# Optimization experiments

Measured on AMD Instinct MI355X. Metric: run time of the kernel, lower is better.

Reference implementation:

```python
import jax, jax.numpy as jnp
import numpy as np

B, D = 8, 256
N_LIVE, K_NEW = 10000, 32
KC = N_LIVE + K_NEW
N_SAMPLES = 100
EPSILON = 0.1


def setup_inputs() -> dict:
    key = jax.random.key(0)
    k1, k2, k3, k4, k5, k6 = jax.random.split(key, 6)
    return {
        "xt": jax.random.normal(k1, (B, D), dtype=jnp.float32),
        "live_x0": jax.random.normal(k2, (B, N_LIVE, D), dtype=jnp.float32),
        "live_ll": jax.random.normal(k3, (B, N_LIVE, 1), dtype=jnp.float32),
        "x0": jax.random.normal(k4, (B, K_NEW, D), dtype=jnp.float32),
        "ll": jax.random.normal(k5, (B, K_NEW, 1), dtype=jnp.float32),
        "t_scale": jnp.float32(0.5),
        "boot_idx": jax.random.randint(k6, (N_SAMPLES, B, KC), 0, KC, dtype=jnp.int32),
    }


def reference(xt, live_x0, live_ll, x0, ll, t_scale, boot_idx):
    # --- spotlight_score core math ---
    # gaussian correction for the new particles: 0.5*||x0-xt||^2/sigma^2 + log(sigma)
    diff_new = x0 - xt[:, None, :]                                   # [B,K,D]
    corr_new = 0.5 * jnp.sum(diff_new ** 2, axis=-1, keepdims=True) / t_scale ** 2  # [B,K,1]
    current_x0 = jnp.concatenate([live_x0, x0], axis=1)              # [B,Kc,D]
    current_ll = jnp.concatenate(
        [live_ll, ll + corr_new + jnp.log(t_scale)], axis=1)         # [B,Kc,1]

    diff = current_x0 - xt[:, None, :]                               # [B,Kc,D]
    use_ll = (current_ll
              - 0.5 * jnp.sum(diff ** 2, axis=-1, keepdims=True) / t_scale ** 2
              - jnp.log(t_scale))                                    # [B,Kc,1]

    scores_p = diff / t_scale                                        # [B,Kc,D] per-particle scores
    logits = use_ll[..., 0]                                          # [B,Kc]

    # --- check_convergence: bootstrap resampled softmax reductions ---
    def body(carry, idx_n):                                          # idx_n: [B,Kc]
        s = jnp.take_along_axis(scores_p, idx_n[:, :, None], axis=1)  # [B,Kc,D]
        l = jnp.take_along_axis(logits, idx_n, axis=1)                # [B,Kc]
        w = jax.nn.softmax(l, axis=1)
        return carry, jnp.einsum('bk,bkd->bd', w, s)                  # [B,D]

    _, boot = jax.lax.scan(body, None, boot_idx)                      # [N,B,D]
    sigma_v = jnp.std(boot, axis=0, ddof=1)                           # [B,D] (torch.std is unbiased)
    converged = jnp.all(sigma_v < EPSILON * t_scale, axis=1)          # [B]

    # --- final importance-weighted score ---
    w = jax.nn.softmax(logits, axis=1)                                # [B,Kc]
    score = jnp.einsum('bk,bkd->bd', w, scores_p)                     # [B,D]
    return score, converged
```

## Files before the change

kernel.cpp:

```cpp
#include <hip/hip_runtime.h>
#include <math.h>

#define B 8
#define D 256
#define N_LIVE 10000
#define K_NEW 32
#define KC 10032
#define NS 100
#define NROW 101
#define EPS 0.1f
#define CAP 1024
#define ACT_CUT 87.0f
#define LBLK 314
#define BMAX_STRIDE 320

#define WS_HDR    0
#define WS_BMAX   160
#define WS_LOGITS (WS_BMAX + B * BMAX_STRIDE)
#define WS_ACTE   (WS_LOGITS + B * KC)
#define WS_ACTI   (WS_ACTE + B * CAP)
#define WS_LUT    (WS_ACTI + B * CAP)
#define WS_BOOT   (WS_LUT + B * KC / 2)

__global__ __launch_bounds__(256) void k_logits(
    const float* __restrict__ xt, const float* __restrict__ live_x0,
    const float* __restrict__ live_ll, const float* __restrict__ x0n,
    const float* __restrict__ lln, const float* __restrict__ ts_p,
    float* __restrict__ logits, float* __restrict__ bmax) {
  int b = blockIdx.y;
  int w = threadIdx.x >> 6;
  int lane = threadIdx.x & 63;
  int k0 = blockIdx.x * 32 + w * 8;
  bool valid = (k0 < KC);
  int kb = valid ? k0 : 0;
  float4 c = ((const float4*)(xt + b * D))[lane];

  float s[8];
#pragma unroll
  for (int p = 0; p < 8; p++) {
    int k = kb + p;
    const float* src = (k < N_LIVE)
        ? (live_x0 + ((size_t)b * N_LIVE + k) * D)
        : (x0n + ((size_t)b * K_NEW + (k - N_LIVE)) * D);
    float4 v = ((const float4*)src)[lane];
    float dx = v.x - c.x, dy = v.y - c.y, dz = v.z - c.z, dw = v.w - c.w;
    s[p] = dx * dx + dy * dy + dz * dz + dw * dw;
  }
#pragma unroll
  for (int off = 32; off; off >>= 1) {
#pragma unroll
    for (int p = 0; p < 8; p++) s[p] += __shfl_xor(s[p], off);
  }
  __shared__ float wlog[4];
  if (lane == 0) {
    float ts = *ts_p;
    float inv2 = 0.5f / (ts * ts), lts = logf(ts);
    float o[8];
#pragma unroll
    for (int p = 0; p < 8; p++) {
      int k = kb + p;
      o[p] = (k < N_LIVE)
          ? live_ll[(size_t)b * N_LIVE + k] - s[p] * inv2 - lts
          : lln[(size_t)b * K_NEW + (k - N_LIVE)];
    }
    if (valid) {
      float4 o0 = {o[0], o[1], o[2], o[3]}, o1 = {o[4], o[5], o[6], o[7]};
      *(float4*)(logits + (size_t)b * KC + kb) = o0;
      *(float4*)(logits + (size_t)b * KC + kb + 4) = o1;
      float m = fmaxf(fmaxf(fmaxf(o[0], o[1]), fmaxf(o[2], o[3])),
                      fmaxf(fmaxf(o[4], o[5]), fmaxf(o[6], o[7])));
      wlog[w] = m;
    } else {
      wlog[w] = -INFINITY;
    }
  }
  __syncthreads();
  if (threadIdx.x == 0)
    bmax[b * BMAX_STRIDE + blockIdx.x] =
        fmaxf(fmaxf(wlog[0], wlog[1]), fmaxf(wlog[2], wlog[3]));
}

__global__ __launch_bounds__(256) void k_bmax(
    const float* __restrict__ bmax, float* __restrict__ hdr) {
  int b = blockIdx.x;
  int tid = threadIdx.x;
  float m = -INFINITY;
  for (int i = tid; i < LBLK; i += 256) m = fmaxf(m, bmax[b * BMAX_STRIDE + i]);
#pragma unroll
  for (int off = 32; off; off >>= 1) m = fmaxf(m, __shfl_xor(m, off));
  __shared__ float sm[4];
  if ((tid & 63) == 0) sm[tid >> 6] = m;
  __syncthreads();
  if (tid == 0)
    hdr[b * 16] = fmaxf(fmaxf(sm[0], sm[1]), fmaxf(sm[2], sm[3]));
}

__global__ __launch_bounds__(256) void k_select(
    const float* __restrict__ logits, const float* __restrict__ hdrM,
    unsigned* __restrict__ hdr, float* __restrict__ act_e,
    int* __restrict__ act_idx, unsigned short* __restrict__ lut) {
  int b = blockIdx.y;
  int tid = blockIdx.x * 256 + threadIdx.x;
  float M = hdrM[b * 16];
  const float* lg = logits + (size_t)b * KC;
  int* cnt = (int*)&hdr[128 + b];
  for (int k = tid; k < KC; k += 8 * 256) {
    float l = lg[k];
    unsigned short v = 0;
    if (l > M - ACT_CUT) {
      int pos = atomicAdd(cnt, 1);
      if (pos < CAP) {
        act_e[b * CAP + pos] = expf(l - M);
        act_idx[b * CAP + pos] = k;
        v = (unsigned short)(pos + 1);
      }
    }
    lut[(size_t)b * KC + k] = v;
  }
}

__global__ __launch_bounds__(256) void k_boot(
    const float* __restrict__ live_x0, const float* __restrict__ x0n,
    const float* __restrict__ act_e, const int* __restrict__ act_idx,
    const unsigned* __restrict__ hdr, const unsigned short* __restrict__ lut,
    const int* __restrict__ boot_idx, float* __restrict__ boot) {
  int n = blockIdx.x;
  int b = blockIdx.y;
  int tid = threadIdx.x;
  int nw = tid >> 6, lane = tid & 63;
  __shared__ int cnt[CAP];
  __shared__ float wval[CAP];
  __shared__ int widx[CAP];
  __shared__ float4 part[4][64];
  __shared__ int snnz;
  __shared__ float sden[4];
  int A = min((int)hdr[128 + b], CAP);
  for (int i = tid; i < A; i += 256) cnt[i] = 0;
  if (tid == 0) snnz = 0;
  __syncthreads();

  if (n < NS) {
    const int4* row = (const int4*)(boot_idx + ((size_t)n * B + b) * KC);
    const unsigned short* lutb = lut + (size_t)b * KC;
    for (int k = tid; k < KC / 4; k += 256) {
      int4 v = row[k];
      int t;
      t = lutb[v.x]; if (t) atomicAdd(&cnt[t - 1], 1);
      t = lutb[v.y]; if (t) atomicAdd(&cnt[t - 1], 1);
      t = lutb[v.z]; if (t) atomicAdd(&cnt[t - 1], 1);
      t = lutb[v.w]; if (t) atomicAdd(&cnt[t - 1], 1);
    }
  } else {
    for (int i = tid; i < A; i += 256) cnt[i] = 1;
  }
  __syncthreads();

  float dpart = 0.f;
  for (int i = tid; i < A; i += 256) {
    int c = cnt[i];
    if (c) {
      float w = (float)c * act_e[b * CAP + i];
      int pos = atomicAdd(&snnz, 1);
      wval[pos] = w;
      widx[pos] = act_idx[b * CAP + i];
      dpart += w;
    }
  }
#pragma unroll
  for (int off = 32; off; off >>= 1) dpart += __shfl_xor(dpart, off);
  if ((tid & 63) == 0) sden[tid >> 6] = dpart;
  __syncthreads();
  float inv = 1.f / (sden[0] + sden[1] + sden[2] + sden[3]);
  int nnz = snnz;

  const float* lx = live_x0 + (size_t)b * N_LIVE * D;
  const float* nx = x0n + (size_t)b * K_NEW * D;
  float4 a0 = {0.f, 0.f, 0.f, 0.f}, a1 = {0.f, 0.f, 0.f, 0.f};
  int p = nw;
  for (; p + 4 < nnz; p += 8) {
    int j0 = widx[p], j1 = widx[p + 4];
    float w0 = wval[p], w1 = wval[p + 4];
    const float4* r0 = (const float4*)((j0 < N_LIVE) ? (lx + (size_t)j0 * D)
                                                     : (nx + (size_t)(j0 - N_LIVE) * D));
    const float4* r1 = (const float4*)((j1 < N_LIVE) ? (lx + (size_t)j1 * D)
                                                     : (nx + (size_t)(j1 - N_LIVE) * D));
    float4 v0 = r0[lane], v1 = r1[lane];
    a0.x = fmaf(w0, v0.x, a0.x); a0.y = fmaf(w0, v0.y, a0.y);
    a0.z = fmaf(w0, v0.z, a0.z); a0.w = fmaf(w0, v0.w, a0.w);
    a1.x = fmaf(w1, v1.x, a1.x); a1.y = fmaf(w1, v1.y, a1.y);
    a1.z = fmaf(w1, v1.z, a1.z); a1.w = fmaf(w1, v1.w, a1.w);
  }
  if (p < nnz) {
    int j = widx[p];
    float w = wval[p];
    const float4* r = (const float4*)((j < N_LIVE) ? (lx + (size_t)j * D)
                                                   : (nx + (size_t)(j - N_LIVE) * D));
    float4 v = r[lane];
    a0.x = fmaf(w, v.x, a0.x); a0.y = fmaf(w, v.y, a0.y);
    a0.z = fmaf(w, v.z, a0.z); a0.w = fmaf(w, v.w, a0.w);
  }
  a0.x += a1.x; a0.y += a1.y; a0.z += a1.z; a0.w += a1.w;
  part[nw][lane] = a0;
  __syncthreads();
  if (nw == 0) {
    float4 q0 = part[0][lane], q1 = part[1][lane], q2 = part[2][lane], q3 = part[3][lane];
    float4 r;
    r.x = ((q0.x + q1.x) + (q2.x + q3.x)) * inv;
    r.y = ((q0.y + q1.y) + (q2.y + q3.y)) * inv;
    r.z = ((q0.z + q1.z) + (q2.z + q3.z)) * inv;
    r.w = ((q0.w + q1.w) + (q2.w + q3.w)) * inv;
    ((float4*)(boot + ((size_t)b * NROW + n) * D))[lane] = r;
  }
}

__global__ __launch_bounds__(256) void k_final(
    const float* __restrict__ boot, const float* __restrict__ xt,
    const float* __restrict__ ts_p, float* __restrict__ out) {
  int b = blockIdx.x;
  int d = threadIdx.x;
  float ts = *ts_p;
  const float* bb = boot + (size_t)b * NROW * D + d;
  float sum = 0.f;
#pragma unroll 4
  for (int n = 0; n < NS; n++) sum += bb[(size_t)n * D];
  float mean = sum / (float)NS;
  float vs = 0.f;
#pragma unroll 4
  for (int n = 0; n < NS; n++) { float t = bb[(size_t)n * D] - mean; vs += t * t; }
  float sigma_raw = sqrtf(vs / (float)(NS - 1));
  bool ok = (sigma_raw / ts) < (EPS * ts);
  out[(size_t)b * D + d] = (bb[(size_t)NS * D] - xt[(size_t)b * D + d]) / ts;
  unsigned long long m = __ballot(ok);
  __shared__ int wok[4];
  if ((d & 63) == 0) wok[d >> 6] = (m == 0xFFFFFFFFFFFFFFFFull) ? 1 : 0;
  __syncthreads();
  if (d == 0) out[(size_t)B * D + b] = (wok[0] & wok[1] & wok[2] & wok[3]) ? 1.0f : 0.0f;
}

extern "C" void kernel_launch(void* const* d_in, const int* in_sizes, int n_in,
                              void* d_out, int out_size, void* d_ws, size_t ws_size,
                              hipStream_t stream) {
  const float* xt       = (const float*)d_in[0];
  const float* live_x0  = (const float*)d_in[1];
  const float* live_ll  = (const float*)d_in[2];
  const float* x0n      = (const float*)d_in[3];
  const float* lln      = (const float*)d_in[4];
  const float* ts_p     = (const float*)d_in[5];
  const int*   boot_idx = (const int*)d_in[6];
  float* out = (float*)d_out;
  float* ws  = (float*)d_ws;

  float* hdrM              = ws + WS_HDR;
  unsigned* hdr            = (unsigned*)(ws + WS_HDR);
  float* bmax              = ws + WS_BMAX;
  float* logits            = ws + WS_LOGITS;
  float* act_e             = ws + WS_ACTE;
  int*   act_idx           = (int*)(ws + WS_ACTI);
  unsigned short* lut      = (unsigned short*)(ws + WS_LUT);
  float* boot              = ws + WS_BOOT;

  hipMemsetAsync(hdr, 0, 160 * sizeof(unsigned), stream);

  k_logits<<<dim3(LBLK, B), 256, 0, stream>>>(xt, live_x0, live_ll, x0n, lln, ts_p, logits, bmax);
  k_bmax<<<dim3(B), 256, 0, stream>>>(bmax, hdrM);
  k_select<<<dim3(8, B), 256, 0, stream>>>(logits, hdrM, hdr, act_e, act_idx, lut);
  k_boot<<<dim3(NROW, B), 256, 0, stream>>>(live_x0, x0n, act_e, act_idx, hdr, lut, boot_idx, boot);
  k_final<<<dim3(B), 256, 0, stream>>>(boot, xt, ts_p, out);
}
```

Measured before the change: 191.6 us.

## Drop memset and bmax kernel, stage LUT in LDS, widen final reduction

Removes the hipMemsetAsync by zeroing the counter inside k_logits. It also removes k_bmax by having every k_select block recompute the per-batch max from the block maxima. k_boot now copies the per-batch LUT into shared memory before the gather, so the random lookups hit LDS instead of global memory, at the cost of about 20KB more LDS per block. k_final splits the sample loop across 1024 threads with a shared-memory reduction to shorten its serial latency.

```diff
diff --git a/kernel.cpp b/kernel.cpp
--- a/kernel.cpp
+++ b/kernel.cpp
@@ -26,8 +26,10 @@
     const float* __restrict__ xt, const float* __restrict__ live_x0,
     const float* __restrict__ live_ll, const float* __restrict__ x0n,
     const float* __restrict__ lln, const float* __restrict__ ts_p,
-    float* __restrict__ logits, float* __restrict__ bmax) {
+    float* __restrict__ logits, float* __restrict__ bmax,
+    unsigned* __restrict__ hdr) {
   int b = blockIdx.y;
+  if (blockIdx.x == 0 && threadIdx.x == 0) hdr[128 + b] = 0;
   int w = threadIdx.x >> 6;
   int lane = threadIdx.x & 63;
   int k0 = blockIdx.x * 32 + w * 8;
@@ -67,9 +69,8 @@
       float4 o0 = {o[0], o[1], o[2], o[3]}, o1 = {o[4], o[5], o[6], o[7]};
       *(float4*)(logits + (size_t)b * KC + kb) = o0;
       *(float4*)(logits + (size_t)b * KC + kb + 4) = o1;
-      float m = fmaxf(fmaxf(fmaxf(o[0], o[1]), fmaxf(o[2], o[3])),
+      wlog[w] = fmaxf(fmaxf(fmaxf(o[0], o[1]), fmaxf(o[2], o[3])),
                       fmaxf(fmaxf(o[4], o[5]), fmaxf(o[6], o[7])));
-      wlog[w] = m;
     } else {
       wlog[w] = -INFINITY;
     }
@@ -80,28 +81,22 @@
         fmaxf(fmaxf(wlog[0], wlog[1]), fmaxf(wlog[2], wlog[3]));
 }
 
-__global__ __launch_bounds__(256) void k_bmax(
-    const float* __restrict__ bmax, float* __restrict__ hdr) {
-  int b = blockIdx.x;
-  int tid = threadIdx.x;
-  float m = -INFINITY;
-  for (int i = tid; i < LBLK; i += 256) m = fmaxf(m, bmax[b * BMAX_STRIDE + i]);
-#pragma unroll
-  for (int off = 32; off; off >>= 1) m = fmaxf(m, __shfl_xor(m, off));
-  __shared__ float sm[4];
-  if ((tid & 63) == 0) sm[tid >> 6] = m;
-  __syncthreads();
-  if (tid == 0)
-    hdr[b * 16] = fmaxf(fmaxf(sm[0], sm[1]), fmaxf(sm[2], sm[3]));
-}
-
 __global__ __launch_bounds__(256) void k_select(
-    const float* __restrict__ logits, const float* __restrict__ hdrM,
+    const float* __restrict__ logits, const float* __restrict__ bmax,
     unsigned* __restrict__ hdr, float* __restrict__ act_e,
     int* __restrict__ act_idx, unsigned short* __restrict__ lut) {
   int b = blockIdx.y;
+  __shared__ float sm[4];
+  float m = -INFINITY;
+  for (int i = threadIdx.x; i < LBLK; i += 256)
+    m = fmaxf(m, bmax[b * BMAX_STRIDE + i]);
+#pragma unroll
+  for (int off = 32; off; off >>= 1) m = fmaxf(m, __shfl_xor(m, off));
+  if ((threadIdx.x & 63) == 0) sm[threadIdx.x >> 6] = m;
+  __syncthreads();
+  float M = fmaxf(fmaxf(sm[0], sm[1]), fmaxf(sm[2], sm[3]));
+
   int tid = blockIdx.x * 256 + threadIdx.x;
-  float M = hdrM[b * 16];
   const float* lg = logits + (size_t)b * KC;
   int* cnt = (int*)&hdr[128 + b];
   for (int k = tid; k < KC; k += 8 * 256) {
@@ -128,6 +123,7 @@
   int b = blockIdx.y;
   int tid = threadIdx.x;
   int nw = tid >> 6, lane = tid & 63;
+  __shared__ unsigned short slut[KC];
   __shared__ int cnt[CAP];
   __shared__ float wval[CAP];
   __shared__ int widx[CAP];
@@ -137,18 +133,22 @@
   int A = min((int)hdr[128 + b], CAP);
   for (int i = tid; i < A; i += 256) cnt[i] = 0;
   if (tid == 0) snnz = 0;
+  if (n < NS) {
+    const unsigned* src = (const unsigned*)(lut + (size_t)b * KC);
+    unsigned* dst = (unsigned*)slut;
+    for (int i = tid; i < KC / 2; i += 256) dst[i] = src[i];
+  }
   __syncthreads();
 
   if (n < NS) {
     const int4* row = (const int4*)(boot_idx + ((size_t)n * B + b) * KC);
-    const unsigned short* lutb = lut + (size_t)b * KC;
     for (int k = tid; k < KC / 4; k += 256) {
       int4 v = row[k];
       int t;
-      t = lutb[v.x]; if (t) atomicAdd(&cnt[t - 1], 1);
-      t = lutb[v.y]; if (t) atomicAdd(&cnt[t - 1], 1);
-      t = lutb[v.z]; if (t) atomicAdd(&cnt[t - 1], 1);
-      t = lutb[v.w]; if (t) atomicAdd(&cnt[t - 1], 1);
+      t = slut[v.x]; if (t) atomicAdd(&cnt[t - 1], 1);
+      t = slut[v.y]; if (t) atomicAdd(&cnt[t - 1], 1);
+      t = slut[v.z]; if (t) atomicAdd(&cnt[t - 1], 1);
+      t = slut[v.w]; if (t) atomicAdd(&cnt[t - 1], 1);
     }
   } else {
     for (int i = tid; i < A; i += 256) cnt[i] = 1;
@@ -213,28 +213,45 @@
   }
 }
 
-__global__ __launch_bounds__(256) void k_final(
+__global__ __launch_bounds__(1024) void k_final(
     const float* __restrict__ boot, const float* __restrict__ xt,
     const float* __restrict__ ts_p, float* __restrict__ out) {
   int b = blockIdx.x;
-  int d = threadIdx.x;
+  int tid = threadIdx.x;
+  int d = tid & 255;
+  int st = tid >> 8;
   float ts = *ts_p;
   const float* bb = boot + (size_t)b * NROW * D + d;
-  float sum = 0.f;
-#pragma unroll 4
-  for (int n = 0; n < NS; n++) sum += bb[(size_t)n * D];
-  float mean = sum / (float)NS;
+  __shared__ float red[4][256];
+  __shared__ float mrow[256];
+  __shared__ int wok[4];
+  float s = 0.f;
+#pragma unroll 5
+  for (int i = 0; i < 25; i++) s += bb[(size_t)(st + 4 * i) * D];
+  red[st][d] = s;
+  __syncthreads();
+  if (st == 0) mrow[d] = (red[0][d] + red[1][d] + red[2][d] + red[3][d]) / (float)NS;
+  __syncthreads();
+  float mean = mrow[d];
   float vs = 0.f;
-#pragma unroll 4
-  for (int n = 0; n < NS; n++) { float t = bb[(size_t)n * D] - mean; vs += t * t; }
-  float sigma_raw = sqrtf(vs / (float)(NS - 1));
-  bool ok = (sigma_raw / ts) < (EPS * ts);
-  out[(size_t)b * D + d] = (bb[(size_t)NS * D] - xt[(size_t)b * D + d]) / ts;
-  unsigned long long m = __ballot(ok);
-  __shared__ int wok[4];
-  if ((d & 63) == 0) wok[d >> 6] = (m == 0xFFFFFFFFFFFFFFFFull) ? 1 : 0;
-  __syncthreads();
-  if (d == 0) out[(size_t)B * D + b] = (wok[0] & wok[1] & wok[2] & wok[3]) ? 1.0f : 0.0f;
+#pragma unroll 5
+  for (int i = 0; i < 25; i++) {
+    float t = bb[(size_t)(st + 4 * i) * D] - mean;
+    vs += t * t;
+  }
+  red[st][d] = vs;
+  __syncthreads();
+  if (st == 0) {
+    float var = (red[0][d] + red[1][d] + red[2][d] + red[3][d]) / (float)(NS - 1);
+    float sigma_raw = sqrtf(var);
+    bool ok = (sigma_raw / ts) < (EPS * ts);
+    out[(size_t)b * D + d] = (bb[(size_t)NS * D] - xt[(size_t)b * D + d]) / ts;
+    unsigned long long m = __ballot(ok);
+    if ((d & 63) == 0) wok[d >> 6] = (m == 0xFFFFFFFFFFFFFFFFull) ? 1 : 0;
+  }
+  __syncthreads();
+  if (tid == 0)
+    out[(size_t)B * D + b] = (wok[0] & wok[1] & wok[2] & wok[3]) ? 1.0f : 0.0f;
 }
 
 extern "C" void kernel_launch(void* const* d_in, const int* in_sizes, int n_in,
@@ -250,7 +267,6 @@
   float* out = (float*)d_out;
   float* ws  = (float*)d_ws;
 
-  float* hdrM              = ws + WS_HDR;
   unsigned* hdr            = (unsigned*)(ws + WS_HDR);
   float* bmax              = ws + WS_BMAX;
   float* logits            = ws + WS_LOGITS;
@@ -259,11 +275,8 @@
   unsigned short* lut      = (unsigned short*)(ws + WS_LUT);
   float* boot              = ws + WS_BOOT;
 
-  hipMemsetAsync(hdr, 0, 160 * sizeof(unsigned), stream);
-
-  k_logits<<<dim3(LBLK, B), 256, 0, stream>>>(xt, live_x0, live_ll, x0n, lln, ts_p, logits, bmax);
-  k_bmax<<<dim3(B), 256, 0, stream>>>(bmax, hdrM);
-  k_select<<<dim3(8, B), 256, 0, stream>>>(logits, hdrM, hdr, act_e, act_idx, lut);
+  k_logits<<<dim3(LBLK, B), 256, 0, stream>>>(xt, live_x0, live_ll, x0n, lln, ts_p, logits, bmax, hdr);
+  k_select<<<dim3(8, B), 256, 0, stream>>>(logits, bmax, hdr, act_e, act_idx, lut);
   k_boot<<<dim3(NROW, B), 256, 0, stream>>>(live_x0, x0n, act_e, act_idx, hdr, lut, boot_idx, boot);
-  k_final<<<dim3(B), 256, 0, stream>>>(boot, xt, ts_p, out);
-}
+  k_final<<<dim3(B), 1024, 0, stream>>>(boot, xt, ts_p, out);
+}
```

Result: faster. 171.7 us (-10.4%).
